# Kernel tuning notes

Measured on AMD Instinct MI355X. Metric: run time of the kernel, lower is better.

The kernel has to match this reference:

```python
import jax, jax.numpy as jnp
import numpy as np

B, TX, TY = 32, 64, 64
D, H, V = 512, 512, 32000
FORGET_BIAS = 1.0  # TF BasicLSTMCell default


def setup_inputs() -> dict:
    key = jax.random.key(0)
    ks = jax.random.split(key, 8)
    enc_ids = jax.random.randint(ks[0], (B, TX), 0, V, dtype=jnp.int32)
    dec_ids = jax.random.randint(ks[1], (B, TY), 0, V, dtype=jnp.int32)
    len_enc = jax.random.randint(ks[2], (B,), 1, TX + 1, dtype=jnp.int32)
    len_dec = jax.random.randint(ks[3], (B,), 1, TY + 1, dtype=jnp.int32)
    E = jax.random.normal(ks[4], (V, D), dtype=jnp.float32) * 0.05
    enc_W = jax.random.normal(ks[5], (D + H, 4 * H), dtype=jnp.float32) * (1.0 / np.sqrt(D + H))
    dec_W = jax.random.normal(ks[6], (D + H, 4 * H), dtype=jnp.float32) * (1.0 / np.sqrt(D + H))
    proj_W = jax.random.normal(ks[7], (H, V), dtype=jnp.float32) * (1.0 / np.sqrt(H))
    return {
        'encoder_inputs': enc_ids, 'decoder_inputs': dec_ids,
        'length_encoder': len_enc, 'length_decoder': len_dec,
        'E': E, 'enc_W': enc_W, 'enc_b': jnp.zeros((4 * H,), jnp.float32),
        'dec_W': dec_W, 'dec_b': jnp.zeros((4 * H,), jnp.float32),
        'proj_W': proj_W,
    }


def _lstm_scan(x_seq, lengths, W, b, c0, h0):
    """Masked LSTM over x_seq [T,B,D]; mimics tf.nn.dynamic_rnn sequence_length
    semantics (state frozen past each example's length). Returns (c,h,hs)."""
    def step(carry, x):
        c, h, t = carry
        z = jnp.concatenate([x, h], axis=-1) @ W + b  # [B,4H]
        i, j, f, o = jnp.split(z, 4, axis=-1)  # TF BasicLSTMCell gate order
        c_new = c * jax.nn.sigmoid(f + FORGET_BIAS) + jax.nn.sigmoid(i) * jnp.tanh(j)
        h_new = jnp.tanh(c_new) * jax.nn.sigmoid(o)
        m = (t < lengths)[:, None]
        c = jnp.where(m, c_new, c)
        h_out = jnp.where(m, h_new, jnp.zeros_like(h_new))  # emitted output zeroed past length
        h = jnp.where(m, h_new, h)
        return (c, h, t + 1), h_out
    (c, h, _), hs = jax.lax.scan(step, (c0, h0, jnp.int32(0)), x_seq)
    return c, h, hs


def reference(encoder_inputs, decoder_inputs, length_encoder, length_decoder,
              E, enc_W, enc_b, dec_W, dec_b, proj_W):
    b = encoder_inputs.shape[0]
    # Encoder: embed + masked LSTM; keep final state.
    enc_x = E[encoder_inputs].transpose(1, 0, 2)  # [TX,B,D]
    z = jnp.zeros((b, enc_W.shape[1] // 4), jnp.float32)
    c, h, _ = _lstm_scan(enc_x, length_encoder, enc_W, enc_b, z, z)
    # Decoder: teacher-forced LSTM from encoder final state + vocab projection.
    dec_x = E[decoder_inputs].transpose(1, 0, 2)  # [TY,B,D]
    _, _, hs = _lstm_scan(dec_x, length_decoder, dec_W, dec_b, c, h)  # [TY,B,H]
    logits = jnp.einsum('tbh,hv->btv', hs, proj_W)  # [B,TY,V]
    # impute_finished=True zeroes outputs past each sequence length
    mask = (jnp.arange(logits.shape[1])[None, :] < length_decoder[:, None])[:, :, None]
    return jnp.where(mask, logits, 0.0)
```

## Files before the change

### kernel.cpp

```cpp
#include <hip/hip_runtime.h>

typedef unsigned short ushort_t;
typedef __attribute__((ext_vector_type(8))) short short8;
typedef __attribute__((ext_vector_type(4))) float f32x4;

__device__ __forceinline__ ushort_t f2bf(float x) {
  union { float f; unsigned int u; } v; v.f = x;
  unsigned int r = v.u + 0x7fffu + ((v.u >> 16) & 1u);
  return (ushort_t)(r >> 16);
}
__device__ __forceinline__ float bf2f(ushort_t h) {
  union { unsigned int u; float f; } v; v.u = ((unsigned int)h) << 16; return v.f;
}
__device__ __forceinline__ void splitbf(float x, ushort_t& hi, ushort_t& lo) {
  hi = f2bf(x);
  lo = f2bf(x - bf2f(hi));
}
__device__ __forceinline__ float sigm(float x) { return 1.f / (1.f + expf(-x)); }
__device__ __forceinline__ f32x4 mfma16(short8 a, short8 b, f32x4 c) {
  return __builtin_amdgcn_mfma_f32_16x16x32_bf16(a, b, c, 0, 0, 0);
}

__device__ __forceinline__ void gload16(const ushort_t* g, ushort_t* l) {
  __builtin_amdgcn_global_load_lds(
      (const __attribute__((address_space(1))) unsigned int*)g,
      (__attribute__((address_space(3))) unsigned int*)l, 16, 0, 0);
}

#define BAR_NB 64
__device__ __forceinline__ void gridbar(int* __restrict__ flags, int bid,
                                        int bm, int tid, int bar) {
  asm volatile("s_waitcnt vmcnt(0)" ::: "memory");
  __syncthreads();
  if (tid == 0)
    __hip_atomic_store(&flags[bid * 32], bar, __ATOMIC_RELAXED,
                       __HIP_MEMORY_SCOPE_AGENT);
  if (tid < 32) {
    while (__hip_atomic_load(&flags[(2 * tid + bm) * 32], __ATOMIC_RELAXED,
                             __HIP_MEMORY_SCOPE_AGENT) < bar) {}
  }
  __syncthreads();
}

__global__ void __launch_bounds__(256) transpose_split(
    const float* __restrict__ src, int ld, int k0,
    ushort_t* __restrict__ hi, ushort_t* __restrict__ lo) {
  __shared__ float tile[64][65];
  const int n0 = blockIdx.x * 64, kb = blockIdx.y * 64;
  #pragma unroll
  for (int i = 0; i < 16; ++i) {
    int idx = i * 256 + threadIdx.x;
    int kk = idx >> 6, nn = idx & 63;
    tile[kk][nn] = src[(size_t)(k0 + kb + kk) * ld + n0 + nn];
  }
  __syncthreads();
  #pragma unroll
  for (int i = 0; i < 16; ++i) {
    int idx = i * 256 + threadIdx.x;
    int nn = idx >> 6, kk = idx & 63;
    float x = tile[kk][nn];
    ushort_t h, l; splitbf(x, h, l);
    size_t o = (size_t)(n0 + nn) * 512 + kb + kk;
    hi[o] = h; lo[o] = l;
  }
}

__global__ void __launch_bounds__(128) embed_split(
    const int* __restrict__ ids, const float* __restrict__ E,
    ushort_t* __restrict__ Ahi, ushort_t* __restrict__ Alo, int T) {
  const int m = blockIdx.x;
  const int b = m & 31, t = m >> 5;
  const int id = ids[b * T + t];
  float4 v = ((const float4*)(E + (size_t)id * 512))[threadIdx.x];
  ushort_t h0, l0, h1, l1, h2, l2, h3, l3;
  splitbf(v.x, h0, l0); splitbf(v.y, h1, l1);
  splitbf(v.z, h2, l2); splitbf(v.w, h3, l3);
  ushort4 hv = make_ushort4(h0, h1, h2, h3);
  ushort4 lv = make_ushort4(l0, l1, l2, l3);
  ((ushort4*)(Ahi + (size_t)m * 512))[threadIdx.x] = hv;
  ((ushort4*)(Alo + (size_t)m * 512))[threadIdx.x] = lv;
}

template <int MFAST>
__global__ void __launch_bounds__(256, 2) gemm_split_t(
    const ushort_t* __restrict__ Ahi, const ushort_t* __restrict__ Alo,
    const ushort_t* __restrict__ Bhi, const ushort_t* __restrict__ Blo,
    const float* __restrict__ bias, float* __restrict__ C, int M, int N) {
  __shared__ __align__(16) ushort_t lAh[128 * 64];
  __shared__ __align__(16) ushort_t lAl[128 * 64];
  __shared__ __align__(16) ushort_t lBh[128 * 64];
  __shared__ __align__(16) ushort_t lBl[128 * 64];
  const int tid = threadIdx.x;
  const int lane = tid & 63, w = tid >> 6;
  const int wm = (w >> 1) * 64, wn = (w & 1) * 64;
  const int lm = lane & 15, lq = lane >> 4;
  const int m0 = (MFAST ? blockIdx.x : blockIdx.y) * 128;
  const int n0 = (MFAST ? blockIdx.y : blockIdx.x) * 128;

  f32x4 acc[4][4];
  #pragma unroll
  for (int i = 0; i < 4; ++i)
    #pragma unroll
    for (int j = 0; j < 4; ++j)
      acc[i][j] = (f32x4){0.f, 0.f, 0.f, 0.f};

  for (int kc = 0; kc < 8; ++kc) {
    if (kc) __syncthreads();
    #pragma unroll
    for (int i = 0; i < 4; ++i) {
      int cid = i * 256 + tid;
      int r = cid >> 3, cl = cid & 7;
      int csrc = cl ^ (r & 7);
      size_t goffA = (size_t)(m0 + r) * 512 + kc * 64 + csrc * 8;
      size_t goffB = (size_t)(n0 + r) * 512 + kc * 64 + csrc * 8;
      int ldso = (i * 256 + w * 64) * 8;
      gload16(Ahi + goffA, lAh + ldso);
      gload16(Alo + goffA, lAl + ldso);
      gload16(Bhi + goffB, lBh + ldso);
      gload16(Blo + goffB, lBl + ldso);
    }
    __syncthreads();
    #pragma unroll
    for (int ks = 0; ks < 2; ++ks) {
      short8 ah[4], al[4], bh[4], bl[4];
      #pragma unroll
      for (int t = 0; t < 4; ++t) {
        int ra = wm + t * 16 + lm;
        int ca = (ks * 4 + lq) ^ (ra & 7);
        ah[t] = *(const short8*)&lAh[ra * 64 + ca * 8];
        al[t] = *(const short8*)&lAl[ra * 64 + ca * 8];
        int rb = wn + t * 16 + lm;
        int cb = (ks * 4 + lq) ^ (rb & 7);
        bh[t] = *(const short8*)&lBh[rb * 64 + cb * 8];
        bl[t] = *(const short8*)&lBl[rb * 64 + cb * 8];
      }
      #pragma unroll
      for (int mt = 0; mt < 4; ++mt)
        #pragma unroll
        for (int nt = 0; nt < 4; ++nt) {
          acc[mt][nt] = mfma16(ah[mt], bh[nt], acc[mt][nt]);
          acc[mt][nt] = mfma16(ah[mt], bl[nt], acc[mt][nt]);
          acc[mt][nt] = mfma16(al[mt], bh[nt], acc[mt][nt]);
        }
    }
  }
  #pragma unroll
  for (int nt = 0; nt < 4; ++nt) {
    int col = n0 + wn + nt * 16 + lm;
    float bv = bias ? bias[col] : 0.f;
    #pragma unroll
    for (int mt = 0; mt < 4; ++mt) {
      int rbase = m0 + wm + mt * 16 + lq * 4;
      #pragma unroll
      for (int r = 0; r < 4; ++r)
        C[(size_t)(rbase + r) * N + col] = acc[mt][nt][r] + bv;
    }
  }
}

__global__ void __launch_bounds__(256, 1) lstm_recurrence(
    const ushort_t* __restrict__ eWh_hi, const ushort_t* __restrict__ eWh_lo,
    const ushort_t* __restrict__ dWh_hi, const ushort_t* __restrict__ dWh_lo,
    const float* __restrict__ xz_enc, const float* __restrict__ xz_dec,
    const int* __restrict__ len_enc, const int* __restrict__ len_dec,
    ushort_t* __restrict__ hseq_hi, ushort_t* __restrict__ hseq_lo,
    ushort_t* __restrict__ hs_hi, ushort_t* __restrict__ hs_lo,
    int* __restrict__ flags) {
  const int tid = threadIdx.x;
  const int lane = tid & 63, g = tid >> 6;
  const int lm = lane & 15, lq = lane >> 4;
  const int bm = blockIdx.x & 1, jg = blockIdx.x >> 1;

  __shared__ float z_x[4][16][17];
  __shared__ float c_st[16][17], h_st[16][17];

  const int bl = tid >> 4, nn = tid & 15;
  const int bglob = bm * 16 + bl;
  const int hcol = jg * 16 + nn;

  c_st[bl][nn] = 0.f; h_st[bl][nn] = 0.f;
  __hip_atomic_store(&hseq_hi[bglob * 512 + hcol], (ushort_t)0,
                     __ATOMIC_RELAXED, __HIP_MEMORY_SCOPE_AGENT);
  __hip_atomic_store(&hseq_lo[bglob * 512 + hcol], (ushort_t)0,
                     __ATOMIC_RELAXED, __HIP_MEMORY_SCOPE_AGENT);
  const int lenE = len_enc[bglob], lenD = len_dec[bglob];

  short8 fbh[16], fbl[16];
  const size_t browoff = (size_t)(g * 512 + jg * 16 + lm) * 512 + lq * 8;
  #pragma unroll
  for (int ks = 0; ks < 16; ++ks) {
    fbh[ks] = *(const short8*)(eWh_hi + browoff + ks * 32);
    fbl[ks] = *(const short8*)(eWh_lo + browoff + ks * 32);
  }

  float pzi, pzj, pzf, pzo;
  {
    const size_t base = (size_t)bglob * 2048 + jg * 16 + nn;
    pzi = xz_enc[base];        pzj = xz_enc[base + 512];
    pzf = xz_enc[base + 1024]; pzo = xz_enc[base + 1536];
  }
  gridbar(flags, blockIdx.x, bm, tid, 1);

  const size_t arow = (size_t)(bm * 16 + lm) * 512 + lq * 8;

  #pragma unroll 1
  for (int s = 0; s < 128; ++s) {
    if (s == 64) {
      #pragma unroll
      for (int ks = 0; ks < 16; ++ks) {
        fbh[ks] = *(const short8*)(dWh_hi + browoff + ks * 32);
        fbl[ks] = *(const short8*)(dWh_lo + browoff + ks * 32);
      }
    }
    const ushort_t* hh = hseq_hi + (size_t)s * 16384;
    const ushort_t* hl = hseq_lo + (size_t)s * 16384;
    ushort_t* ohh = hseq_hi + (size_t)(s + 1) * 16384;
    ushort_t* ohl = hseq_lo + (size_t)(s + 1) * 16384;

    f32x4 a0 = (f32x4){0.f, 0.f, 0.f, 0.f};
    f32x4 a1 = (f32x4){0.f, 0.f, 0.f, 0.f};
    f32x4 a2 = (f32x4){0.f, 0.f, 0.f, 0.f};
    #pragma unroll
    for (int ks = 0; ks < 16; ++ks) {
      short8 ah = *(const short8*)(hh + arow + ks * 32);
      short8 al = *(const short8*)(hl + arow + ks * 32);
      a0 = mfma16(ah, fbh[ks], a0);
      a1 = mfma16(ah, fbl[ks], a1);
      a2 = mfma16(al, fbh[ks], a2);
    }
    #pragma unroll
    for (int r = 0; r < 4; ++r)
      z_x[g][lq * 4 + r][lm] = a0[r] + a1[r] + a2[r];
    __syncthreads();

    {
      const bool isdec = s >= 64;
      const int t = isdec ? s - 64 : s;
      const int len = isdec ? lenD : lenE;
      float zi = z_x[0][bl][nn] + pzi;
      float zj = z_x[1][bl][nn] + pzj;
      float zf = z_x[2][bl][nn] + pzf;
      float zo = z_x[3][bl][nn] + pzo;
      float co = c_st[bl][nn], ho = h_st[bl][nn];
      float cn = co * sigm(zf + 1.0f) + sigm(zi) * tanhf(zj);
      float hn = tanhf(cn) * sigm(zo);
      bool msk = t < len;
      float ck = msk ? cn : co;
      float hk = msk ? hn : ho;
      c_st[bl][nn] = ck; h_st[bl][nn] = hk;
      ushort_t hi, lo;
      splitbf(hk, hi, lo);
      __hip_atomic_store(&ohh[bglob * 512 + hcol], hi, __ATOMIC_RELAXED,
                         __HIP_MEMORY_SCOPE_AGENT);
      __hip_atomic_store(&ohl[bglob * 512 + hcol], lo, __ATOMIC_RELAXED,
                         __HIP_MEMORY_SCOPE_AGENT);
      if (isdec) {
        float hv = msk ? hn : 0.f;
        splitbf(hv, hi, lo);
        hs_hi[((size_t)bglob * 64 + t) * 512 + hcol] = hi;
        hs_lo[((size_t)bglob * 64 + t) * 512 + hcol] = lo;
      }
    }
    if (s != 127) {
      const int sp = s + 1;
      const bool pd = sp >= 64;
      const float* xz = pd ? xz_dec : xz_enc;
      const int tp = pd ? sp - 64 : sp;
      const size_t base = ((size_t)tp * 32 + bglob) * 2048 + jg * 16 + nn;
      pzi = xz[base];        pzj = xz[base + 512];
      pzf = xz[base + 1024]; pzo = xz[base + 1536];
      gridbar(flags, blockIdx.x, bm, tid, s + 2);
    }
  }
}

extern "C" void kernel_launch(void* const* d_in, const int* in_sizes, int n_in,
                              void* d_out, int out_size, void* d_ws, size_t ws_size,
                              hipStream_t stream) {
  (void)in_sizes; (void)n_in; (void)out_size; (void)ws_size;
  const int*   enc_ids = (const int*)d_in[0];
  const int*   dec_ids = (const int*)d_in[1];
  const int*   len_enc = (const int*)d_in[2];
  const int*   len_dec = (const int*)d_in[3];
  const float* E       = (const float*)d_in[4];
  const float* enc_W   = (const float*)d_in[5];
  const float* enc_b   = (const float*)d_in[6];
  const float* dec_W   = (const float*)d_in[7];
  const float* dec_b   = (const float*)d_in[8];
  const float* proj_W  = (const float*)d_in[9];

  char* w = (char*)d_ws;
  auto carve = [&](size_t bytes) -> char* {
    char* p = w; w += (bytes + 255) & ~(size_t)255; return p;
  };
  const size_t WSZ = 2048 * 512 * 2;
  ushort_t* eWx_hi = (ushort_t*)carve(WSZ); ushort_t* eWx_lo = (ushort_t*)carve(WSZ);
  ushort_t* eWh_hi = (ushort_t*)carve(WSZ); ushort_t* eWh_lo = (ushort_t*)carve(WSZ);
  ushort_t* dWx_hi = (ushort_t*)carve(WSZ); ushort_t* dWx_lo = (ushort_t*)carve(WSZ);
  ushort_t* dWh_hi = (ushort_t*)carve(WSZ); ushort_t* dWh_lo = (ushort_t*)carve(WSZ);
  ushort_t* pW_hi  = (ushort_t*)carve((size_t)32000 * 512 * 2);
  ushort_t* pW_lo  = (ushort_t*)carve((size_t)32000 * 512 * 2);
  ushort_t* Ae_hi  = (ushort_t*)carve(WSZ); ushort_t* Ae_lo = (ushort_t*)carve(WSZ);
  ushort_t* Ad_hi  = (ushort_t*)carve(WSZ); ushort_t* Ad_lo = (ushort_t*)carve(WSZ);
  float* xz_enc = (float*)carve((size_t)64 * 32 * 2048 * 4);
  float* xz_dec = (float*)carve((size_t)64 * 32 * 2048 * 4);
  ushort_t* hs_hi = (ushort_t*)carve(WSZ); ushort_t* hs_lo = (ushort_t*)carve(WSZ);
  ushort_t* hseq_hi = (ushort_t*)carve((size_t)129 * 32 * 512 * 2);
  ushort_t* hseq_lo = (ushort_t*)carve((size_t)129 * 32 * 512 * 2);
  int* flags = (int*)carve(BAR_NB * 32 * sizeof(int));

  dim3 blk(256);
  transpose_split<<<dim3(32, 8),  blk, 0, stream>>>(enc_W, 2048, 0,   eWx_hi, eWx_lo);
  transpose_split<<<dim3(32, 8),  blk, 0, stream>>>(enc_W, 2048, 512, eWh_hi, eWh_lo);
  transpose_split<<<dim3(32, 8),  blk, 0, stream>>>(dec_W, 2048, 0,   dWx_hi, dWx_lo);
  transpose_split<<<dim3(32, 8),  blk, 0, stream>>>(dec_W, 2048, 512, dWh_hi, dWh_lo);
  transpose_split<<<dim3(500, 8), blk, 0, stream>>>(proj_W, 32000, 0, pW_hi, pW_lo);

  embed_split<<<2048, 128, 0, stream>>>(enc_ids, E, Ae_hi, Ae_lo, 64);
  embed_split<<<2048, 128, 0, stream>>>(dec_ids, E, Ad_hi, Ad_lo, 64);

  gemm_split_t<0><<<dim3(16, 16), blk, 0, stream>>>(Ae_hi, Ae_lo, eWx_hi, eWx_lo,
                                                    enc_b, xz_enc, 2048, 2048);
  gemm_split_t<0><<<dim3(16, 16), blk, 0, stream>>>(Ad_hi, Ad_lo, dWx_hi, dWx_lo,
                                                    dec_b, xz_dec, 2048, 2048);

  void* args[] = { &eWh_hi, &eWh_lo, &dWh_hi, &dWh_lo,
                   (void*)&xz_enc, (void*)&xz_dec,
                   (void*)&len_enc, (void*)&len_dec,
                   &hseq_hi, &hseq_lo, &hs_hi, &hs_lo, &flags };
  hipLaunchCooperativeKernel((void*)lstm_recurrence, dim3(64), dim3(256),
                             args, 0, stream);

  const float* nobias = nullptr;
  gemm_split_t<1><<<dim3(16, 250), blk, 0, stream>>>(hs_hi, hs_lo, pW_hi, pW_lo,
                                                     nobias, (float*)d_out,
                                                     2048, 32000);
}
```

Measured before the change: 1.514 ms.

## Switch non-recurrent GEMMs to single-pass fp16 and use counter-based grid barrier

Replaces the three-MFMA bf16 hi/lo split GEMMs (input projections and the vocab projection) with single fp16 MFMA GEMMs, using fp16 copies of the weights, embeddings and decoder outputs. This cuts MFMA work by about a factor of three and halves operand memory traffic. It also replaces the per-block flag barrier with an atomic counter per barrier instance, which needs a zeroing kernel first. Precision drops from roughly fp32-equivalent to fp16 with fp32 accumulation, which may exceed tolerance.

```diff
diff --git a/kernel.cpp b/kernel.cpp
--- a/kernel.cpp
+++ b/kernel.cpp
@@ -1,7 +1,10 @@
 #include <hip/hip_runtime.h>
 
 typedef unsigned short ushort_t;
+typedef _Float16 half_t;
 typedef __attribute__((ext_vector_type(8))) short short8;
+typedef __attribute__((ext_vector_type(8))) _Float16 half8;
+typedef __attribute__((ext_vector_type(4))) _Float16 half4;
 typedef __attribute__((ext_vector_type(4))) float f32x4;
 
 __device__ __forceinline__ ushort_t f2bf(float x) {
@@ -20,26 +23,32 @@
 __device__ __forceinline__ f32x4 mfma16(short8 a, short8 b, f32x4 c) {
   return __builtin_amdgcn_mfma_f32_16x16x32_bf16(a, b, c, 0, 0, 0);
 }
-
-__device__ __forceinline__ void gload16(const ushort_t* g, ushort_t* l) {
+__device__ __forceinline__ f32x4 mfma16h(half8 a, half8 b, f32x4 c) {
+  return __builtin_amdgcn_mfma_f32_16x16x32_f16(a, b, c, 0, 0, 0);
+}
+
+__device__ __forceinline__ void gload16(const void* g, void* l) {
   __builtin_amdgcn_global_load_lds(
       (const __attribute__((address_space(1))) unsigned int*)g,
       (__attribute__((address_space(3))) unsigned int*)l, 16, 0, 0);
 }
 
-#define BAR_NB 64
-__device__ __forceinline__ void gridbar(int* __restrict__ flags, int bid,
-                                        int bm, int tid, int bar) {
+__device__ __forceinline__ void gridbar_cnt(int* __restrict__ cnt, int bm,
+                                            int tid, int bar) {
   asm volatile("s_waitcnt vmcnt(0)" ::: "memory");
   __syncthreads();
-  if (tid == 0)
-    __hip_atomic_store(&flags[bid * 32], bar, __ATOMIC_RELAXED,
-                       __HIP_MEMORY_SCOPE_AGENT);
-  if (tid < 32) {
-    while (__hip_atomic_load(&flags[(2 * tid + bm) * 32], __ATOMIC_RELAXED,
-                             __HIP_MEMORY_SCOPE_AGENT) < bar) {}
+  if (tid == 0) {
+    int* p = &cnt[(bar * 2 + bm) * 32];
+    __hip_atomic_fetch_add(p, 1, __ATOMIC_RELAXED, __HIP_MEMORY_SCOPE_AGENT);
+    while (__hip_atomic_load(p, __ATOMIC_RELAXED,
+                             __HIP_MEMORY_SCOPE_AGENT) < 32) {}
   }
   __syncthreads();
+}
+
+__global__ void zero_ints(int* __restrict__ p, int n) {
+  for (int i = blockIdx.x * 256 + threadIdx.x; i < n; i += gridDim.x * 256)
+    p[i] = 0;
 }
 
 __global__ void __launch_bounds__(256) transpose_split(
@@ -65,37 +74,46 @@
   }
 }
 
-__global__ void __launch_bounds__(128) embed_split(
+__global__ void __launch_bounds__(256) transpose_f16(
+    const float* __restrict__ src, int ld, int k0, half_t* __restrict__ dst) {
+  __shared__ float tile[64][65];
+  const int n0 = blockIdx.x * 64, kb = blockIdx.y * 64;
+  #pragma unroll
+  for (int i = 0; i < 16; ++i) {
+    int idx = i * 256 + threadIdx.x;
+    int kk = idx >> 6, nn = idx & 63;
+    tile[kk][nn] = src[(size_t)(k0 + kb + kk) * ld + n0 + nn];
+  }
+  __syncthreads();
+  #pragma unroll
+  for (int i = 0; i < 16; ++i) {
+    int idx = i * 256 + threadIdx.x;
+    int nn = idx >> 6, kk = idx & 63;
+    dst[(size_t)(n0 + nn) * 512 + kb + kk] = (half_t)tile[kk][nn];
+  }
+}
+
+__global__ void __launch_bounds__(128) embed_f16(
     const int* __restrict__ ids, const float* __restrict__ E,
-    ushort_t* __restrict__ Ahi, ushort_t* __restrict__ Alo, int T) {
+    half_t* __restrict__ A, int T) {
   const int m = blockIdx.x;
   const int b = m & 31, t = m >> 5;
   const int id = ids[b * T + t];
   float4 v = ((const float4*)(E + (size_t)id * 512))[threadIdx.x];
-  ushort_t h0, l0, h1, l1, h2, l2, h3, l3;
-  splitbf(v.x, h0, l0); splitbf(v.y, h1, l1);
-  splitbf(v.z, h2, l2); splitbf(v.w, h3, l3);
-  ushort4 hv = make_ushort4(h0, h1, h2, h3);
-  ushort4 lv = make_ushort4(l0, l1, l2, l3);
-  ((ushort4*)(Ahi + (size_t)m * 512))[threadIdx.x] = hv;
-  ((ushort4*)(Alo + (size_t)m * 512))[threadIdx.x] = lv;
-}
-
-template <int MFAST>
-__global__ void __launch_bounds__(256, 2) gemm_split_t(
-    const ushort_t* __restrict__ Ahi, const ushort_t* __restrict__ Alo,
-    const ushort_t* __restrict__ Bhi, const ushort_t* __restrict__ Blo,
-    const float* __restrict__ bias, float* __restrict__ C, int M, int N) {
-  __shared__ __align__(16) ushort_t lAh[128 * 64];
-  __shared__ __align__(16) ushort_t lAl[128 * 64];
-  __shared__ __align__(16) ushort_t lBh[128 * 64];
-  __shared__ __align__(16) ushort_t lBl[128 * 64];
+  half4 h = {(half_t)v.x, (half_t)v.y, (half_t)v.z, (half_t)v.w};
+  ((half4*)(A + (size_t)m * 512))[threadIdx.x] = h;
+}
+
+__global__ void __launch_bounds__(256, 2) gemm_f16(
+    const half_t* __restrict__ A, const half_t* __restrict__ Bm,
+    const float* __restrict__ bias, float* __restrict__ C, int N) {
+  __shared__ __align__(16) half_t lA[128 * 64];
+  __shared__ __align__(16) half_t lB[128 * 64];
   const int tid = threadIdx.x;
   const int lane = tid & 63, w = tid >> 6;
   const int wm = (w >> 1) * 64, wn = (w & 1) * 64;
   const int lm = lane & 15, lq = lane >> 4;
-  const int m0 = (MFAST ? blockIdx.x : blockIdx.y) * 128;
-  const int n0 = (MFAST ? blockIdx.y : blockIdx.x) * 128;
+  const int m0 = blockIdx.x * 128, n0 = blockIdx.y * 128;
 
   f32x4 acc[4][4];
   #pragma unroll
@@ -114,34 +132,27 @@
       size_t goffA = (size_t)(m0 + r) * 512 + kc * 64 + csrc * 8;
       size_t goffB = (size_t)(n0 + r) * 512 + kc * 64 + csrc * 8;
       int ldso = (i * 256 + w * 64) * 8;
-      gload16(Ahi + goffA, lAh + ldso);
-      gload16(Alo + goffA, lAl + ldso);
-      gload16(Bhi + goffB, lBh + ldso);
-      gload16(Blo + goffB, lBl + ldso);
+      gload16(A + goffA, lA + ldso);
+      gload16(Bm + goffB, lB + ldso);
     }
     __syncthreads();
     #pragma unroll
     for (int ks = 0; ks < 2; ++ks) {
-      short8 ah[4], al[4], bh[4], bl[4];
+      half8 a[4], b[4];
       #pragma unroll
       for (int t = 0; t < 4; ++t) {
         int ra = wm + t * 16 + lm;
         int ca = (ks * 4 + lq) ^ (ra & 7);
-        ah[t] = *(const short8*)&lAh[ra * 64 + ca * 8];
-        al[t] = *(const short8*)&lAl[ra * 64 + ca * 8];
+        a[t] = *(const half8*)&lA[ra * 64 + ca * 8];
         int rb = wn + t * 16 + lm;
         int cb = (ks * 4 + lq) ^ (rb & 7);
-        bh[t] = *(const short8*)&lBh[rb * 64 + cb * 8];
-        bl[t] = *(const short8*)&lBl[rb * 64 + cb * 8];
+        b[t] = *(const half8*)&lB[rb * 64 + cb * 8];
       }
       #pragma unroll
       for (int mt = 0; mt < 4; ++mt)
         #pragma unroll
-        for (int nt = 0; nt < 4; ++nt) {
-          acc[mt][nt] = mfma16(ah[mt], bh[nt], acc[mt][nt]);
-          acc[mt][nt] = mfma16(ah[mt], bl[nt], acc[mt][nt]);
-          acc[mt][nt] = mfma16(al[mt], bh[nt], acc[mt][nt]);
-        }
+        for (int nt = 0; nt < 4; ++nt)
+          acc[mt][nt] = mfma16h(a[mt], b[nt], acc[mt][nt]);
     }
   }
   #pragma unroll
@@ -164,8 +175,7 @@
     const float* __restrict__ xz_enc, const float* __restrict__ xz_dec,
     const int* __restrict__ len_enc, const int* __restrict__ len_dec,
     ushort_t* __restrict__ hseq_hi, ushort_t* __restrict__ hseq_lo,
-    ushort_t* __restrict__ hs_hi, ushort_t* __restrict__ hs_lo,
-    int* __restrict__ flags) {
+    half_t* __restrict__ hs_f16, int* __restrict__ cnt) {
   const int tid = threadIdx.x;
   const int lane = tid & 63, g = tid >> 6;
   const int lm = lane & 15, lq = lane >> 4;
@@ -199,7 +209,7 @@
     pzi = xz_enc[base];        pzj = xz_enc[base + 512];
     pzf = xz_enc[base + 1024]; pzo = xz_enc[base + 1536];
   }
-  gridbar(flags, blockIdx.x, bm, tid, 1);
+  gridbar_cnt(cnt, bm, tid, 1);
 
   const size_t arow = (size_t)(bm * 16 + lm) * 512 + lq * 8;
 
@@ -256,9 +266,7 @@
                          __HIP_MEMORY_SCOPE_AGENT);
       if (isdec) {
         float hv = msk ? hn : 0.f;
-        splitbf(hv, hi, lo);
-        hs_hi[((size_t)bglob * 64 + t) * 512 + hcol] = hi;
-        hs_lo[((size_t)bglob * 64 + t) * 512 + hcol] = lo;
+        hs_f16[((size_t)bglob * 64 + t) * 512 + hcol] = (half_t)hv;
       }
     }
     if (s != 127) {
@@ -269,7 +277,7 @@
       const size_t base = ((size_t)tp * 32 + bglob) * 2048 + jg * 16 + nn;
       pzi = xz[base];        pzj = xz[base + 512];
       pzf = xz[base + 1024]; pzo = xz[base + 1536];
-      gridbar(flags, blockIdx.x, bm, tid, s + 2);
+      gridbar_cnt(cnt, bm, tid, s + 2);
     }
   }
 }
@@ -294,45 +302,44 @@
     char* p = w; w += (bytes + 255) & ~(size_t)255; return p;
   };
   const size_t WSZ = 2048 * 512 * 2;
-  ushort_t* eWx_hi = (ushort_t*)carve(WSZ); ushort_t* eWx_lo = (ushort_t*)carve(WSZ);
   ushort_t* eWh_hi = (ushort_t*)carve(WSZ); ushort_t* eWh_lo = (ushort_t*)carve(WSZ);
-  ushort_t* dWx_hi = (ushort_t*)carve(WSZ); ushort_t* dWx_lo = (ushort_t*)carve(WSZ);
   ushort_t* dWh_hi = (ushort_t*)carve(WSZ); ushort_t* dWh_lo = (ushort_t*)carve(WSZ);
-  ushort_t* pW_hi  = (ushort_t*)carve((size_t)32000 * 512 * 2);
-  ushort_t* pW_lo  = (ushort_t*)carve((size_t)32000 * 512 * 2);
-  ushort_t* Ae_hi  = (ushort_t*)carve(WSZ); ushort_t* Ae_lo = (ushort_t*)carve(WSZ);
-  ushort_t* Ad_hi  = (ushort_t*)carve(WSZ); ushort_t* Ad_lo = (ushort_t*)carve(WSZ);
+  half_t*   eWxf   = (half_t*)carve(WSZ);
+  half_t*   dWxf   = (half_t*)carve(WSZ);
+  half_t*   pWf    = (half_t*)carve((size_t)32000 * 512 * 2);
+  half_t*   Aef    = (half_t*)carve(WSZ);
+  half_t*   Adf    = (half_t*)carve(WSZ);
   float* xz_enc = (float*)carve((size_t)64 * 32 * 2048 * 4);
   float* xz_dec = (float*)carve((size_t)64 * 32 * 2048 * 4);
-  ushort_t* hs_hi = (ushort_t*)carve(WSZ); ushort_t* hs_lo = (ushort_t*)carve(WSZ);
+  half_t* hs_f16 = (half_t*)carve(WSZ);
   ushort_t* hseq_hi = (ushort_t*)carve((size_t)129 * 32 * 512 * 2);
   ushort_t* hseq_lo = (ushort_t*)carve((size_t)129 * 32 * 512 * 2);
-  int* flags = (int*)carve(BAR_NB * 32 * sizeof(int));
+  const int NCNT = 260 * 32;
+  int* cnt = (int*)carve(NCNT * sizeof(int));
 
   dim3 blk(256);
-  transpose_split<<<dim3(32, 8),  blk, 0, stream>>>(enc_W, 2048, 0,   eWx_hi, eWx_lo);
+  zero_ints<<<33, 256, 0, stream>>>(cnt, NCNT);
+
   transpose_split<<<dim3(32, 8),  blk, 0, stream>>>(enc_W, 2048, 512, eWh_hi, eWh_lo);
-  transpose_split<<<dim3(32, 8),  blk, 0, stream>>>(dec_W, 2048, 0,   dWx_hi, dWx_lo);
   transpose_split<<<dim3(32, 8),  blk, 0, stream>>>(dec_W, 2048, 512, dWh_hi, dWh_lo);
-  transpose_split<<<dim3(500, 8), blk, 0, stream>>>(proj_W, 32000, 0, pW_hi, pW_lo);
-
-  embed_split<<<2048, 128, 0, stream>>>(enc_ids, E, Ae_hi, Ae_lo, 64);
-  embed_split<<<2048, 128, 0, stream>>>(dec_ids, E, Ad_hi, Ad_lo, 64);
-
-  gemm_split_t<0><<<dim3(16, 16), blk, 0, stream>>>(Ae_hi, Ae_lo, eWx_hi, eWx_lo,
-                                                    enc_b, xz_enc, 2048, 2048);
-  gemm_split_t<0><<<dim3(16, 16), blk, 0, stream>>>(Ad_hi, Ad_lo, dWx_hi, dWx_lo,
-                                                    dec_b, xz_dec, 2048, 2048);
+  transpose_f16<<<dim3(32, 8),    blk, 0, stream>>>(enc_W, 2048, 0, eWxf);
+  transpose_f16<<<dim3(32, 8),    blk, 0, stream>>>(dec_W, 2048, 0, dWxf);
+  transpose_f16<<<dim3(500, 8),   blk, 0, stream>>>(proj_W, 32000, 0, pWf);
+
+  embed_f16<<<2048, 128, 0, stream>>>(enc_ids, E, Aef, 64);
+  embed_f16<<<2048, 128, 0, stream>>>(dec_ids, E, Adf, 64);
+
+  gemm_f16<<<dim3(16, 16), blk, 0, stream>>>(Aef, eWxf, enc_b, xz_enc, 2048);
+  gemm_f16<<<dim3(16, 16), blk, 0, stream>>>(Adf, dWxf, dec_b, xz_dec, 2048);
 
   void* args[] = { &eWh_hi, &eWh_lo, &dWh_hi, &dWh_lo,
                    (void*)&xz_enc, (void*)&xz_dec,
                    (void*)&len_enc, (void*)&len_dec,
-                   &hseq_hi, &hseq_lo, &hs_hi, &hs_lo, &flags };
+                   &hseq_hi, &hseq_lo, &hs_f16, &cnt };
   hipLaunchCooperativeKernel((void*)lstm_recurrence, dim3(64), dim3(256),
                              args, 0, stream);
 
   const float* nobias = nullptr;
-  gemm_split_t<1><<<dim3(16, 250), blk, 0, stream>>>(hs_hi, hs_lo, pW_hi, pW_lo,
-                                                     nobias, (float*)d_out,
-                                                     2048, 32000);
-}
+  gemm_f16<<<dim3(16, 250), blk, 0, stream>>>(hs_f16, pWf, nobias,
+                                              (float*)d_out, 32000);
+}
```

After: 1.470 ms. -2.9%, faster.
